# Performance work log

Hardware: AMD Instinct MI355X
Metric: run time of the kernel (lower is better)

## Reference

```python
import jax, jax.numpy as jnp
import numpy as np

N = 21  # nodes per graph (20 laser sectors + 1 robot node)
MAX_RANGE = 10.0
_bound = np.linspace(-np.pi / 2 - 0.03, np.pi / 2, 21, dtype=np.float32)[:-1]
_angles = _bound + np.float32(np.pi / 20)
ANGLE_FEAT = jnp.asarray(np.stack([np.sin(_angles), np.cos(_angles)], 1), dtype=jnp.float32)  # [20,2]


def _build_nodes(state24):
    # state24: [B,24] -> node features [B,21,7]
    B = state24.shape[0]
    laser = state24[:, :20, None] / MAX_RANGE                       # [B,20,1]
    angle = jnp.broadcast_to(ANGLE_FEAT[None], (B, 20, 2))          # [B,20,2]
    sector = jnp.concatenate([laser, angle, jnp.zeros((B, 20, 4), state24.dtype)], -1)  # [B,20,7]
    robot = jnp.concatenate([jnp.zeros((B, 1, 3), state24.dtype), state24[:, None, 20:]], -1)  # [B,1,7]
    return jnp.concatenate([sector, robot], axis=1)                 # [B,21,7]


def _gatv2(x, Wl, Wr, att, bias, heads, dim):
    # GATv2 over a fully-connected graph with self-loops (dense all-pairs).
    # e_ij = att . leaky_relu(Wl x_j + Wr x_i); alpha = softmax_j; out_i = sum_j alpha_ij (Wl x_j)
    B = x.shape[0]
    gl = (x @ Wl).reshape(B, N, heads, dim)  # source transform [B,j,H,D]
    gr = (x @ Wr).reshape(B, N, heads, dim)  # target transform [B,i,H,D]
    s = jax.nn.leaky_relu(gl[:, None] + gr[:, :, None], negative_slope=0.2)  # [B,i,j,H,D]
    e = jnp.einsum('bijhd,hd->bijh', s, att)                                  # [B,i,j,H]
    alpha = jax.nn.softmax(e, axis=2)                                          # softmax over sources j
    out = jnp.einsum('bijh,bjhd->bihd', alpha, gl).reshape(B, N, heads * dim)
    return out + bias


def setup_inputs() -> dict:
    key = jax.random.key(0)
    ks = jax.random.split(key, 16)
    r = lambda k, shape, s: (jax.random.normal(k, shape, dtype=jnp.float32) * s)
    B = 1024
    return {
        'state24': jax.random.normal(ks[0], (B, 24), dtype=jnp.float32),
        'Wl1': r(ks[1], (7, 256), 0.3), 'Wr1': r(ks[2], (7, 256), 0.3),
        'att1': r(ks[3], (4, 64), 0.1), 'b1': r(ks[4], (256,), 0.02),
        'Wl2': r(ks[5], (256, 64), 0.06), 'Wr2': r(ks[6], (256, 64), 0.06),
        'att2': r(ks[7], (1, 64), 0.1), 'b2': r(ks[8], (64,), 0.02),
        'fc1_w': r(ks[9], (64, 256), 0.12), 'fc1_b': r(ks[10], (256,), 0.02),
        'fc2_w': r(ks[11], (256, 256), 0.06), 'fc2_b': r(ks[12], (256,), 0.02),
        'fc3_w': r(ks[13], (256, 2), 0.06), 'fc3_b': r(ks[14], (2,), 0.02),
    }


def reference(state24, Wl1, Wr1, att1, b1, Wl2, Wr2, att2, b2,
              fc1_w, fc1_b, fc2_w, fc2_b, fc3_w, fc3_b):
    x = _build_nodes(state24)                               # [B,21,7]
    h = jax.nn.elu(_gatv2(x, Wl1, Wr1, att1, b1, 4, 64))    # [B,21,256]
    h = _gatv2(h, Wl2, Wr2, att2, b2, 1, 64)                # [B,21,64]
    nfv = jnp.mean(h, axis=1)                               # global_mean_pool -> [B,64]
    h = jax.nn.relu(nfv @ fc1_w + fc1_b)
    h = jax.nn.relu(h @ fc2_w + fc2_b)
    return jnp.tanh(h @ fc3_w + fc3_b)                      # [B,2]
```

## Files before the change

kernel.cpp:

```cpp
#include <hip/hip_runtime.h>
#include <hip/hip_fp16.h>
#include <math.h>

#define PI_D 3.141592653589793

typedef _Float16 h2 __attribute__((ext_vector_type(2)));
typedef _Float16 h4 __attribute__((ext_vector_type(4)));
typedef _Float16 h8 __attribute__((ext_vector_type(8)));
typedef unsigned short us8 __attribute__((ext_vector_type(8)));
typedef __fp16 f16v2 __attribute__((ext_vector_type(2)));
typedef __fp16 f16v8 __attribute__((ext_vector_type(8)));
typedef float f32x4 __attribute__((ext_vector_type(4)));

#define STR1 264
#define STR2H 72

static __device__ __forceinline__ h2 pack_h2(float a, float b) {
    return __builtin_bit_cast(h2, __builtin_amdgcn_cvt_pkrtz(a, b));
}

static __device__ __forceinline__ float fdot2(h2 a, h2 b, float c) {
    return __builtin_amdgcn_fdot2(__builtin_bit_cast(f16v2, a),
                                  __builtin_bit_cast(f16v2, b), c, false);
}

static __device__ __forceinline__ h8 habs8(h8 x) {
    us8 u = __builtin_bit_cast(us8, x);
    us8 m = {0x7fff, 0x7fff, 0x7fff, 0x7fff, 0x7fff, 0x7fff, 0x7fff, 0x7fff};
    return __builtin_bit_cast(h8, (us8)(u & m));
}

static __device__ __forceinline__ f32x4 mfma16(h8 a, h8 b, f32x4 c) {
    return __builtin_amdgcn_mfma_f32_16x16x32_f16(
        __builtin_bit_cast(f16v8, a), __builtin_bit_cast(f16v8, b), c, 0, 0, 0);
}

__global__ __launch_bounds__(256) void pack_weights_kernel(
    const float* __restrict__ Wl2, const float* __restrict__ Wr2,
    const float* __restrict__ fc1_w, const float* __restrict__ fc2_w,
    h8* __restrict__ ws)
{
    int idx = blockIdx.x * 256 + threadIdx.x;
    if (idx < 4096) {
        const float* W = idx < 2048 ? Wl2 : Wr2;
        int t = idx & 2047;
        int ntile = t >> 9, rem = t & 511;
        int kchunk = rem >> 6, lane = rem & 63;
        int n = ntile * 16 + (lane & 15);
        int k0 = kchunk * 32 + (lane >> 4) * 8;
        h8 o;
        #pragma unroll
        for (int j = 0; j < 8; ++j) o[j] = (_Float16)W[(k0 + j) * 64 + n];
        ws[idx] = o;
    } else if (idx < 6144) {
        int t = idx - 4096;
        int k2 = t >> 6, c = t & 63;
        h8 o;
        #pragma unroll
        for (int q = 0; q < 4; ++q) {
            o[2 * q]     = (_Float16)fc1_w[(2 * k2) * 256 + 4 * c + q];
            o[2 * q + 1] = (_Float16)fc1_w[(2 * k2 + 1) * 256 + 4 * c + q];
        }
        ws[idx] = o;
    } else {
        int t = idx - 6144;
        int k2 = t >> 6, c = t & 63;
        h8 o;
        #pragma unroll
        for (int q = 0; q < 4; ++q) {
            o[2 * q]     = (_Float16)fc2_w[(2 * k2) * 256 + 4 * c + q];
            o[2 * q + 1] = (_Float16)fc2_w[(2 * k2 + 1) * 256 + 4 * c + q];
        }
        ws[idx] = o;
    }
}

__global__ __launch_bounds__(256, 4) void actor_fused_kernel(
    const float* __restrict__ state24,
    const float* __restrict__ Wl1, const float* __restrict__ Wr1,
    const float* __restrict__ att1, const float* __restrict__ b1,
    const float* __restrict__ att2, const float* __restrict__ b2,
    const float* __restrict__ fc1_b, const float* __restrict__ fc2_b,
    const float* __restrict__ fc3_w, const float* __restrict__ fc3_b,
    const h8* __restrict__ wsL, const h8* __restrict__ wsR,
    const h8* __restrict__ wsF1, const h8* __restrict__ wsF2,
    float* __restrict__ out, int B)
{
    const int bix = blockIdx.x;
    if (bix >= B) return;
    const int tid = threadIdx.x;

    __shared__ float sinL[20], cosL[20], laserL[20], robotL[4];
    __shared__ __align__(16) h2 attLh[128];
    __shared__ __align__(16) h2 att2Lh[32];
    __shared__ __align__(16) _Float16 gr1h[22 * STR1];
    __shared__ __align__(16) union {
        struct { _Float16 gl1h[22 * STR1];
                 float ePf[128 * 24];
                 float uv[168]; } p1;
        struct { _Float16 gl2h[21 * STR2H];
                 _Float16 gr2h[21 * STR2H];
                 _Float16 gl2hT[64 * 32];
                 float e2[32 * 24];
                 float u2v2[42];
                 float red[4][256];
                 _Float16 nfvh[64]; _Float16 hah[256]; _Float16 hbh[256]; } p2;
    } U;

    if (tid < 20) {
        double step = (PI_D + 0.03) / 20.0;
        float bound = (float)(-PI_D / 2.0 - 0.03 + (double)tid * step);
        float ang = bound + (float)(PI_D / 20.0);
        sinL[tid] = sinf(ang);
        cosL[tid] = cosf(ang);
        laserL[tid] = state24[bix * 24 + tid] * 0.1f;
    }
    if (tid >= 32 && tid < 36) robotL[tid - 32] = state24[bix * 24 + 20 + (tid - 32)];
    if (tid < 128) {
        float2 ap = ((const float2*)att1)[tid];
        attLh[tid] = pack_h2(0.4f * ap.x, 0.4f * ap.y);
    }
    if (tid >= 128 && tid < 160) {
        float2 ap = ((const float2*)att2)[tid - 128];
        att2Lh[tid - 128] = pack_h2(0.4f * ap.x, 0.4f * ap.y);
    }
    __syncthreads();

    {
        h8 zz = {};
        if (tid < 33) ((h8*)U.p1.gl1h)[21 * 33 + tid] = zz;

        const int d2 = tid & 127;
        const int half = tid >> 7;
        float2 wl[7], wr[7];
        #pragma unroll
        for (int k = 0; k < 7; k++) {
            wl[k] = ((const float2*)Wl1)[k * 128 + d2];
            wr[k] = ((const float2*)Wr1)[k * 128 + d2];
        }
        const int base = half * 11;
        #pragma unroll
        for (int nn = 0; nn < 11; ++nn) {
            int node = base + nn;
            if (node < 21) {
                float a0, a1, b0, b1v;
                if (node < 20) {
                    float l = laserL[node], s = sinL[node], c = cosL[node];
                    a0 = l * wl[0].x + s * wl[1].x + c * wl[2].x;
                    a1 = l * wl[0].y + s * wl[1].y + c * wl[2].y;
                    b0 = l * wr[0].x + s * wr[1].x + c * wr[2].x;
                    b1v = l * wr[0].y + s * wr[1].y + c * wr[2].y;
                } else {
                    float r0 = robotL[0], r1 = robotL[1], r2 = robotL[2], r3 = robotL[3];
                    a0 = r0 * wl[3].x + r1 * wl[4].x + r2 * wl[5].x + r3 * wl[6].x;
                    a1 = r0 * wl[3].y + r1 * wl[4].y + r2 * wl[5].y + r3 * wl[6].y;
                    b0 = r0 * wr[3].x + r1 * wr[4].x + r2 * wr[5].x + r3 * wr[6].x;
                    b1v = r0 * wr[3].y + r1 * wr[4].y + r2 * wr[5].y + r3 * wr[6].y;
                }
                ((h2*)(U.p1.gl1h + node * STR1))[d2] = pack_h2(a0, a1);
                ((h2*)(gr1h + node * STR1))[d2] = pack_h2(b0, b1v);
            }
        }
    }
    __syncthreads();

    if (tid < 168) {
        int r = tid < 84 ? tid : tid - 84;
        int h = r / 21, idx = r - h * 21;
        const _Float16* rowp = (tid < 84 ? U.p1.gl1h : gr1h) + idx * STR1 + h * 64;
        const h8* row8 = (const h8*)rowp;
        const h2* ar = attLh + h * 32;
        float l0 = 0.f, l1 = 0.f;
        #pragma unroll
        for (int ch = 0; ch < 8; ++ch) {
            h8 g = row8[ch];
            l0 = fdot2(__builtin_shufflevector(g, g, 0, 1), ar[ch * 4 + 0], l0);
            l1 = fdot2(__builtin_shufflevector(g, g, 2, 3), ar[ch * 4 + 1], l1);
            l0 = fdot2(__builtin_shufflevector(g, g, 4, 5), ar[ch * 4 + 2], l0);
            l1 = fdot2(__builtin_shufflevector(g, g, 6, 7), ar[ch * 4 + 3], l1);
        }
        U.p1.uv[tid] = l0 + l1;
    }
    __syncthreads();

    {
        const int h = tid >> 6;
        const int lane = tid & 63;
        h2 ar[32];
        #pragma unroll
        for (int q = 0; q < 32; ++q) ar[q] = attLh[h * 32 + q];

        for (int it = 0; it < 7; ++it) {
            int q = it * 64 + lane;
            if (q < 441) {
                int i = q / 21;
                int j = q - i * 21;
                const h8* gA8 = (const h8*)(U.p1.gl1h + j * STR1 + h * 64);
                const h8* gB8 = (const h8*)(gr1h + i * STR1 + h * 64);
                float m0 = 0.f, m1 = 0.f;
                #pragma unroll
                for (int ch = 0; ch < 8; ++ch) {
                    h8 x = gA8[ch] + gB8[ch];
                    h8 ax = habs8(x);
                    m0 = fdot2(__builtin_shufflevector(ax, ax, 0, 1), ar[ch * 4 + 0], m0);
                    m1 = fdot2(__builtin_shufflevector(ax, ax, 2, 3), ar[ch * 4 + 1], m1);
                    m0 = fdot2(__builtin_shufflevector(ax, ax, 4, 5), ar[ch * 4 + 2], m0);
                    m1 = fdot2(__builtin_shufflevector(ax, ax, 6, 7), ar[ch * 4 + 3], m1);
                }
                U.p1.ePf[(h * 32 + i) * 24 + j] = m0 + m1;
            }
        }
    }
    __syncthreads();

    if (tid < 84) {
        int h = tid / 21, i = tid - h * 21;
        int r = h * 32 + i;
        float* row = U.p1.ePf + r * 24;
        const float* uu = U.p1.uv + h * 21;
        float vi = 1.5f * U.p1.uv[84 + h * 21 + i];
        float ebuf[21];
        float m = -1e30f;
        #pragma unroll
        for (int j = 0; j < 21; j++) {
            float e = row[j] + 1.5f * uu[j] + vi;
            ebuf[j] = e;
            m = fmaxf(m, e);
        }
        float s = 0.f;
        #pragma unroll
        for (int j = 0; j < 21; j++) { float v = __expf(ebuf[j] - m); ebuf[j] = v; s += v; }
        float rinv = 1.f / s;
        h8* hp8 = (h8*)(U.p1.ePf) + r * 6;
        h8 o0, o1, o2;
        #pragma unroll
        for (int q = 0; q < 8; ++q) o0[q] = (_Float16)(ebuf[q] * rinv);
        #pragma unroll
        for (int q = 0; q < 8; ++q) o1[q] = (_Float16)(ebuf[8 + q] * rinv);
        #pragma unroll
        for (int q = 0; q < 5; ++q) o2[q] = (_Float16)(ebuf[16 + q] * rinv);
        o2[5] = (_Float16)0.f; o2[6] = (_Float16)0.f; o2[7] = (_Float16)0.f;
        h8 zz = {};
        hp8[0] = o0; hp8[1] = o1; hp8[2] = o2;
        hp8[3] = zz; hp8[4] = zz; hp8[5] = zz;
    } else {
        h8 zz = {};
        for (int z = tid - 84; z < 264; z += 172) {
            int rr = z / 6, slot = z - rr * 6;
            int h = rr / 11, m = 21 + (rr - h * 11);
            ((h8*)U.p1.ePf)[(h * 32 + m) * 6 + slot] = zz;
        }
    }
    __syncthreads();

    {
        h8 zz = {};
        if (tid < 33) ((h8*)gr1h)[21 * 33 + tid] = zz;

        const int lane = tid & 63;
        const int h = tid >> 6;
        const int mcol = lane & 15;
        const int quad = lane >> 4;
        const h8* Af = (const h8*)U.p1.ePf;
        h8 A0 = Af[(h * 32 + mcol) * 6 + quad];
        h8 A1 = Af[(h * 32 + 16 + mcol) * 6 + quad];
        int rowoff[8];
        #pragma unroll
        for (int jj = 0; jj < 8; ++jj) {
            int rr = quad * 8 + jj;
            rowoff[jj] = (rr > 21 ? 21 : rr) * STR1;
        }
        const int colbase = h * 64 + mcol;
        f32x4 z4 = {0.f, 0.f, 0.f, 0.f};
        #pragma unroll
        for (int t = 0; t < 4; ++t) {
            int col = colbase + t * 16;
            h8 bv;
            #pragma unroll
            for (int jj = 0; jj < 8; ++jj) bv[jj] = U.p1.gl1h[rowoff[jj] + col];
            f32x4 d0 = mfma16(A0, bv, z4);
            f32x4 d1 = mfma16(A1, bv, z4);
            float bb = b1[col];
            #pragma unroll
            for (int r = 0; r < 4; ++r) {
                int n0 = quad * 4 + r;
                float v = d0[r] + bb;
                v = v > 0.f ? v : __expf(v) - 1.f;
                gr1h[n0 * STR1 + col] = (_Float16)v;
                int n1 = 16 + quad * 4 + r;
                if (n1 < 21) {
                    float w2 = d1[r] + bb;
                    w2 = w2 > 0.f ? w2 : __expf(w2) - 1.f;
                    gr1h[n1 * STR1 + col] = (_Float16)w2;
                }
            }
        }
    }
    __syncthreads();

    {
        const int lane = tid & 63;
        const int w = tid >> 6;
        const int mrow = lane & 15;
        const int quad = lane >> 4;
        int rowA1 = 16 + mrow; if (rowA1 > 21) rowA1 = 21;
        const h8* hA0 = (const h8*)(gr1h + mrow * STR1 + quad * 8);
        const h8* hA1 = (const h8*)(gr1h + rowA1 * STR1 + quad * 8);
        const h8* bL = wsL + w * 512 + lane;
        const h8* bR = wsR + w * 512 + lane;
        f32x4 aL0 = {0.f, 0.f, 0.f, 0.f}, aL1 = {0.f, 0.f, 0.f, 0.f};
        f32x4 aR0 = {0.f, 0.f, 0.f, 0.f}, aR1 = {0.f, 0.f, 0.f, 0.f};
        #pragma unroll
        for (int kc = 0; kc < 8; ++kc) {
            h8 A0 = hA0[kc * 4];
            h8 A1 = hA1[kc * 4];
            h8 BL = bL[kc * 64];
            h8 BR = bR[kc * 64];
            aL0 = mfma16(A0, BL, aL0);
            aL1 = mfma16(A1, BL, aL1);
            aR0 = mfma16(A0, BR, aR0);
            aR1 = mfma16(A1, BR, aR1);
        }
        const int col = w * 16 + mrow;
        #pragma unroll
        for (int r = 0; r < 4; ++r) {
            int row0 = quad * 4 + r;
            U.p2.gl2h[row0 * STR2H + col] = (_Float16)aL0[r];
            U.p2.gr2h[row0 * STR2H + col] = (_Float16)aR0[r];
            int row1 = 16 + row0;
            if (row1 < 21) {
                U.p2.gl2h[row1 * STR2H + col] = (_Float16)aL1[r];
                U.p2.gr2h[row1 * STR2H + col] = (_Float16)aR1[r];
            }
        }
        {
            h2 lo0 = pack_h2(aL0[0], aL0[1]);
            h2 hi0 = pack_h2(aL0[2], aL0[3]);
            h4 p0 = __builtin_shufflevector(lo0, hi0, 0, 1, 2, 3);
            *(h4*)(U.p2.gl2hT + col * 32 + quad * 4) = p0;
            float m0v = (16 + quad * 4 + 0 < 21) ? aL1[0] : 0.f;
            float m1v = (16 + quad * 4 + 1 < 21) ? aL1[1] : 0.f;
            float m2v = (16 + quad * 4 + 2 < 21) ? aL1[2] : 0.f;
            float m3v = (16 + quad * 4 + 3 < 21) ? aL1[3] : 0.f;
            h2 lo1 = pack_h2(m0v, m1v);
            h2 hi1 = pack_h2(m2v, m3v);
            h4 p1 = __builtin_shufflevector(lo1, hi1, 0, 1, 2, 3);
            *(h4*)(U.p2.gl2hT + col * 32 + 16 + quad * 4) = p1;
        }
    }
    __syncthreads();

    {
        h2 ar2[32];
        #pragma unroll
        for (int q = 0; q < 32; ++q) ar2[q] = att2Lh[q];

        #pragma unroll
        for (int it = 0; it < 2; ++it) {
            int t = it * 256 + tid;
            if (t < 441) {
                int i = t / 21;
                int j = t - i * 21;
                const h8* gA8 = (const h8*)(U.p2.gl2h + j * STR2H);
                const h8* gB8 = (const h8*)(U.p2.gr2h + i * STR2H);
                float m0 = 0.f, m1 = 0.f;
                #pragma unroll
                for (int ch = 0; ch < 8; ++ch) {
                    h8 x = gA8[ch] + gB8[ch];
                    h8 ax = habs8(x);
                    m0 = fdot2(__builtin_shufflevector(ax, ax, 0, 1), ar2[ch * 4 + 0], m0);
                    m1 = fdot2(__builtin_shufflevector(ax, ax, 2, 3), ar2[ch * 4 + 1], m1);
                    m0 = fdot2(__builtin_shufflevector(ax, ax, 4, 5), ar2[ch * 4 + 2], m0);
                    m1 = fdot2(__builtin_shufflevector(ax, ax, 6, 7), ar2[ch * 4 + 3], m1);
                }
                U.p2.e2[i * 24 + j] = m0 + m1;
            } else if (t < 483) {
                int u = t - 441;
                int r = u < 21 ? u : u - 21;
                const _Float16* rowp = (u < 21 ? U.p2.gl2h : U.p2.gr2h) + r * STR2H;
                const h8* row8 = (const h8*)rowp;
                float l0 = 0.f, l1 = 0.f;
                #pragma unroll
                for (int ch = 0; ch < 8; ++ch) {
                    h8 g = row8[ch];
                    l0 = fdot2(__builtin_shufflevector(g, g, 0, 1), ar2[ch * 4 + 0], l0);
                    l1 = fdot2(__builtin_shufflevector(g, g, 2, 3), ar2[ch * 4 + 1], l1);
                    l0 = fdot2(__builtin_shufflevector(g, g, 4, 5), ar2[ch * 4 + 2], l0);
                    l1 = fdot2(__builtin_shufflevector(g, g, 6, 7), ar2[ch * 4 + 3], l1);
                }
                U.p2.u2v2[u] = l0 + l1;
            }
        }
    }
    __syncthreads();

    if (tid < 21) {
        float* row = U.p2.e2 + tid * 24;
        const float* uu = U.p2.u2v2;
        float vi = 1.5f * U.p2.u2v2[21 + tid];
        float ebuf[21];
        float m = -1e30f;
        #pragma unroll
        for (int j = 0; j < 21; j++) {
            float e = row[j] + 1.5f * uu[j] + vi;
            ebuf[j] = e;
            m = fmaxf(m, e);
        }
        float s = 0.f;
        #pragma unroll
        for (int j = 0; j < 21; j++) { float v = __expf(ebuf[j] - m); ebuf[j] = v; s += v; }
        float rinv = 1.f / s;
        h8* hp8 = (h8*)(U.p2.e2) + tid * 6;
        h8 o0, o1, o2;
        #pragma unroll
        for (int q = 0; q < 8; ++q) o0[q] = (_Float16)(ebuf[q] * rinv);
        #pragma unroll
        for (int q = 0; q < 8; ++q) o1[q] = (_Float16)(ebuf[8 + q] * rinv);
        #pragma unroll
        for (int q = 0; q < 5; ++q) o2[q] = (_Float16)(ebuf[16 + q] * rinv);
        o2[5] = (_Float16)0.f; o2[6] = (_Float16)0.f; o2[7] = (_Float16)0.f;
        h8 zz = {};
        hp8[0] = o0; hp8[1] = o1; hp8[2] = o2;
        hp8[3] = zz; hp8[4] = zz; hp8[5] = zz;
    } else if (tid < 87) {
        int z = tid - 21;
        int rr = z / 6, slot = z - rr * 6;
        h8 zz = {};
        ((h8*)U.p2.e2)[(21 + rr) * 6 + slot] = zz;
    }
    __syncthreads();

    {
        const int lane = tid & 63;
        const int w = tid >> 6;
        const int mcol = lane & 15;
        const int quad = lane >> 4;
        const h8* Af2 = (const h8*)U.p2.e2;
        h8 A0 = Af2[mcol * 6 + quad];
        h8 A1 = Af2[(16 + mcol) * 6 + quad];
        h8 bv = *(const h8*)(U.p2.gl2hT + (w * 16 + mcol) * 32 + quad * 8);
        f32x4 z4 = {0.f, 0.f, 0.f, 0.f};
        f32x4 d0 = mfma16(A0, bv, z4);
        f32x4 d1 = mfma16(A1, bv, z4);
        float s = (d0[0] + d0[1]) + (d0[2] + d0[3])
                + (d1[0] + d1[1]) + (d1[2] + d1[3]);
        s += __shfl_xor(s, 16, 64);
        s += __shfl_xor(s, 32, 64);
        if (quad == 0) {
            int col = w * 16 + mcol;
            U.p2.nfvh[col] = (_Float16)(s * (1.f / 21.f) + b2[col]);
        }
    }
    __syncthreads();

    {
        int c = tid & 63, g = tid >> 6;
        const h2* x2p = (const h2*)U.p2.nfvh;
        float4 acc = {0.f, 0.f, 0.f, 0.f};
        #pragma unroll
        for (int kk = 0; kk < 8; ++kk) {
            int k2 = g * 8 + kk;
            h8 w = wsF1[k2 * 64 + c];
            h2 x2 = x2p[k2];
            acc.x = fdot2(__builtin_shufflevector(w, w, 0, 1), x2, acc.x);
            acc.y = fdot2(__builtin_shufflevector(w, w, 2, 3), x2, acc.y);
            acc.z = fdot2(__builtin_shufflevector(w, w, 4, 5), x2, acc.z);
            acc.w = fdot2(__builtin_shufflevector(w, w, 6, 7), x2, acc.w);
        }
        ((float4*)U.p2.red[g])[c] = acc;
    }
    __syncthreads();
    {
        float v = U.p2.red[0][tid] + U.p2.red[1][tid] + U.p2.red[2][tid] + U.p2.red[3][tid]
                  + fc1_b[tid];
        U.p2.hah[tid] = (_Float16)fmaxf(v, 0.f);
    }
    __syncthreads();

    {
        int c = tid & 63, g = tid >> 6;
        const h8* haH = (const h8*)U.p2.hah;
        float4 acc = {0.f, 0.f, 0.f, 0.f};
#define FC2_STEP(q, p)                                                          \
        {                                                                       \
            int k2 = g * 32 + (q) * 4 + (p);                                    \
            h8 w = wsF2[k2 * 64 + c];                                           \
            h2 x2 = __builtin_shufflevector(xa, xa, 2 * (p), 2 * (p) + 1);      \
            acc.x = fdot2(__builtin_shufflevector(w, w, 0, 1), x2, acc.x);      \
            acc.y = fdot2(__builtin_shufflevector(w, w, 2, 3), x2, acc.y);      \
            acc.z = fdot2(__builtin_shufflevector(w, w, 4, 5), x2, acc.z);      \
            acc.w = fdot2(__builtin_shufflevector(w, w, 6, 7), x2, acc.w);      \
        }
        #pragma unroll
        for (int q = 0; q < 8; ++q) {
            h8 xa = haH[g * 8 + q];
            FC2_STEP(q, 0)
            FC2_STEP(q, 1)
            FC2_STEP(q, 2)
            FC2_STEP(q, 3)
        }
#undef FC2_STEP
        ((float4*)U.p2.red[g])[c] = acc;
    }
    __syncthreads();
    {
        float v = U.p2.red[0][tid] + U.p2.red[1][tid] + U.p2.red[2][tid] + U.p2.red[3][tid]
                  + fc2_b[tid];
        U.p2.hbh[tid] = (_Float16)fmaxf(v, 0.f);
    }
    __syncthreads();

    if (tid < 128) {
        int o = tid >> 6, l = tid & 63;
        float s = 0.f;
        #pragma unroll
        for (int m = 0; m < 4; m++) {
            int k = l + 64 * m;
            s = fmaf((float)U.p2.hbh[k], fc3_w[k * 2 + o], s);
        }
        #pragma unroll
        for (int off = 32; off >= 1; off >>= 1) s += __shfl_down(s, off, 64);
        if (l == 0) out[bix * 2 + o] = tanhf(s + fc3_b[o]);
    }
}

extern "C" void kernel_launch(void* const* d_in, const int* in_sizes, int n_in,
                              void* d_out, int out_size, void* d_ws, size_t ws_size,
                              hipStream_t stream) {
    const float* state24 = (const float*)d_in[0];
    const float* Wl1 = (const float*)d_in[1];
    const float* Wr1 = (const float*)d_in[2];
    const float* att1 = (const float*)d_in[3];
    const float* b1 = (const float*)d_in[4];
    const float* Wl2 = (const float*)d_in[5];
    const float* Wr2 = (const float*)d_in[6];
    const float* att2 = (const float*)d_in[7];
    const float* b2 = (const float*)d_in[8];
    const float* fc1_w = (const float*)d_in[9];
    const float* fc1_b = (const float*)d_in[10];
    const float* fc2_w = (const float*)d_in[11];
    const float* fc2_b = (const float*)d_in[12];
    const float* fc3_w = (const float*)d_in[13];
    const float* fc3_b = (const float*)d_in[14];
    float* out = (float*)d_out;

    h8* ws = (h8*)d_ws;
    const h8* wsL = ws;
    const h8* wsR = ws + 2048;
    const h8* wsF1 = ws + 4096;
    const h8* wsF2 = ws + 6144;

    pack_weights_kernel<<<56, 256, 0, stream>>>(Wl2, Wr2, fc1_w, fc2_w, ws);

    int B = in_sizes[0] / 24;
    actor_fused_kernel<<<B, 256, 0, stream>>>(
        state24, Wl1, Wr1, att1, b1, att2, b2,
        fc1_b, fc2_b, fc3_w, fc3_b,
        wsL, wsR, wsF1, wsF2, out, B);
}
```

Before: 115.8 us.

## Restructure GAT layer-1 scoring, prefetch layer-2 weights, and make FC layers per-thread

Layer-1 pairwise attention scores are now computed by giving each lane one target node and seven source nodes, holding the target row in registers. The separate u/v projection pass is merged into the same barrier phase, which removes one __syncthreads. Padding rows are dropped (22→21 rows, 128→84 score rows), so several zero-fill passes go away, and the layer-2 weight fragments are loaded into registers before the MFMA stage. FC1 and FC2 weights are re-laid out so each thread computes one output column over the full K dimension. This removes the cross-group reduction buffer and two barriers, at the cost of more registers and longer per-thread dependency chains.

```diff
diff --git a/kernel.cpp b/kernel.cpp
--- a/kernel.cpp
+++ b/kernel.cpp
@@ -14,6 +14,8 @@
 
 #define STR1 264
 #define STR2H 72
+
+#define SV(v, a, b) __builtin_shufflevector(v, v, a, b)
 
 static __device__ __forceinline__ h2 pack_h2(float a, float b) {
     return __builtin_bit_cast(h2, __builtin_amdgcn_cvt_pkrtz(a, b));
@@ -54,23 +56,17 @@
         ws[idx] = o;
     } else if (idx < 6144) {
         int t = idx - 4096;
-        int k2 = t >> 6, c = t & 63;
+        int col = t >> 3, kk = t & 7;
         h8 o;
         #pragma unroll
-        for (int q = 0; q < 4; ++q) {
-            o[2 * q]     = (_Float16)fc1_w[(2 * k2) * 256 + 4 * c + q];
-            o[2 * q + 1] = (_Float16)fc1_w[(2 * k2 + 1) * 256 + 4 * c + q];
-        }
+        for (int j = 0; j < 8; ++j) o[j] = (_Float16)fc1_w[(kk * 8 + j) * 256 + col];
         ws[idx] = o;
     } else {
         int t = idx - 6144;
-        int k2 = t >> 6, c = t & 63;
+        int col = t >> 5, kk = t & 31;
         h8 o;
         #pragma unroll
-        for (int q = 0; q < 4; ++q) {
-            o[2 * q]     = (_Float16)fc2_w[(2 * k2) * 256 + 4 * c + q];
-            o[2 * q + 1] = (_Float16)fc2_w[(2 * k2 + 1) * 256 + 4 * c + q];
-        }
+        for (int j = 0; j < 8; ++j) o[j] = (_Float16)fc2_w[(kk * 8 + j) * 256 + col];
         ws[idx] = o;
     }
 }
@@ -93,17 +89,16 @@
     __shared__ float sinL[20], cosL[20], laserL[20], robotL[4];
     __shared__ __align__(16) h2 attLh[128];
     __shared__ __align__(16) h2 att2Lh[32];
-    __shared__ __align__(16) _Float16 gr1h[22 * STR1];
+    __shared__ __align__(16) _Float16 gr1h[21 * STR1];
     __shared__ __align__(16) union {
-        struct { _Float16 gl1h[22 * STR1];
-                 float ePf[128 * 24];
+        struct { _Float16 gl1h[21 * STR1];
+                 float ePf[84 * 24];
                  float uv[168]; } p1;
         struct { _Float16 gl2h[21 * STR2H];
                  _Float16 gr2h[21 * STR2H];
                  _Float16 gl2hT[64 * 32];
                  float e2[32 * 24];
                  float u2v2[42];
-                 float red[4][256];
                  _Float16 nfvh[64]; _Float16 hah[256]; _Float16 hbh[256]; } p2;
     } U;
 
@@ -127,9 +122,6 @@
     __syncthreads();
 
     {
-        h8 zz = {};
-        if (tid < 33) ((h8*)U.p1.gl1h)[21 * 33 + tid] = zz;
-
         const int d2 = tid & 127;
         const int half = tid >> 7;
         float2 wl[7], wr[7];
@@ -164,25 +156,6 @@
     }
     __syncthreads();
 
-    if (tid < 168) {
-        int r = tid < 84 ? tid : tid - 84;
-        int h = r / 21, idx = r - h * 21;
-        const _Float16* rowp = (tid < 84 ? U.p1.gl1h : gr1h) + idx * STR1 + h * 64;
-        const h8* row8 = (const h8*)rowp;
-        const h2* ar = attLh + h * 32;
-        float l0 = 0.f, l1 = 0.f;
-        #pragma unroll
-        for (int ch = 0; ch < 8; ++ch) {
-            h8 g = row8[ch];
-            l0 = fdot2(__builtin_shufflevector(g, g, 0, 1), ar[ch * 4 + 0], l0);
-            l1 = fdot2(__builtin_shufflevector(g, g, 2, 3), ar[ch * 4 + 1], l1);
-            l0 = fdot2(__builtin_shufflevector(g, g, 4, 5), ar[ch * 4 + 2], l0);
-            l1 = fdot2(__builtin_shufflevector(g, g, 6, 7), ar[ch * 4 + 3], l1);
-        }
-        U.p1.uv[tid] = l0 + l1;
-    }
-    __syncthreads();
-
     {
         const int h = tid >> 6;
         const int lane = tid & 63;
@@ -190,33 +163,54 @@
         #pragma unroll
         for (int q = 0; q < 32; ++q) ar[q] = attLh[h * 32 + q];
 
-        for (int it = 0; it < 7; ++it) {
-            int q = it * 64 + lane;
-            if (q < 441) {
-                int i = q / 21;
-                int j = q - i * 21;
-                const h8* gA8 = (const h8*)(U.p1.gl1h + j * STR1 + h * 64);
-                const h8* gB8 = (const h8*)(gr1h + i * STR1 + h * 64);
+        if (lane < 63) {
+            const int i = lane / 3;
+            const int jg = lane - i * 3;
+            const h8* gB8 = (const h8*)(gr1h + i * STR1 + h * 64);
+            h8 br[8];
+            #pragma unroll
+            for (int ch = 0; ch < 8; ++ch) br[ch] = gB8[ch];
+            const h8* gA8 = (const h8*)(U.p1.gl1h + (jg * 7) * STR1 + h * 64);
+            float* eo = U.p1.ePf + (h * 21 + i) * 24 + jg * 7;
+            #pragma unroll
+            for (int s = 0; s < 7; ++s) {
                 float m0 = 0.f, m1 = 0.f;
                 #pragma unroll
                 for (int ch = 0; ch < 8; ++ch) {
-                    h8 x = gA8[ch] + gB8[ch];
+                    h8 x = gA8[ch] + br[ch];
                     h8 ax = habs8(x);
-                    m0 = fdot2(__builtin_shufflevector(ax, ax, 0, 1), ar[ch * 4 + 0], m0);
-                    m1 = fdot2(__builtin_shufflevector(ax, ax, 2, 3), ar[ch * 4 + 1], m1);
-                    m0 = fdot2(__builtin_shufflevector(ax, ax, 4, 5), ar[ch * 4 + 2], m0);
-                    m1 = fdot2(__builtin_shufflevector(ax, ax, 6, 7), ar[ch * 4 + 3], m1);
+                    m0 = fdot2(SV(ax, 0, 1), ar[ch * 4 + 0], m0);
+                    m1 = fdot2(SV(ax, 2, 3), ar[ch * 4 + 1], m1);
+                    m0 = fdot2(SV(ax, 4, 5), ar[ch * 4 + 2], m0);
+                    m1 = fdot2(SV(ax, 6, 7), ar[ch * 4 + 3], m1);
                 }
-                U.p1.ePf[(h * 32 + i) * 24 + j] = m0 + m1;
+                eo[s] = m0 + m1;
+                gA8 += 33;
             }
+        }
+        if (tid < 168) {
+            int r = tid < 84 ? tid : tid - 84;
+            int hu = r / 21, idx = r - hu * 21;
+            const _Float16* rowp = (tid < 84 ? U.p1.gl1h : gr1h) + idx * STR1 + hu * 64;
+            const h8* row8 = (const h8*)rowp;
+            const h2* aru = attLh + hu * 32;
+            float l0 = 0.f, l1 = 0.f;
+            #pragma unroll
+            for (int ch = 0; ch < 8; ++ch) {
+                h8 g = row8[ch];
+                l0 = fdot2(SV(g, 0, 1), aru[ch * 4 + 0], l0);
+                l1 = fdot2(SV(g, 2, 3), aru[ch * 4 + 1], l1);
+                l0 = fdot2(SV(g, 4, 5), aru[ch * 4 + 2], l0);
+                l1 = fdot2(SV(g, 6, 7), aru[ch * 4 + 3], l1);
+            }
+            U.p1.uv[tid] = l0 + l1;
         }
     }
     __syncthreads();
 
     if (tid < 84) {
         int h = tid / 21, i = tid - h * 21;
-        int r = h * 32 + i;
-        float* row = U.p1.ePf + r * 24;
+        float* row = U.p1.ePf + tid * 24;
         const float* uu = U.p1.uv + h * 21;
         float vi = 1.5f * U.p1.uv[84 + h * 21 + i];
         float ebuf[21];
@@ -231,7 +225,7 @@
         #pragma unroll
         for (int j = 0; j < 21; j++) { float v = __expf(ebuf[j] - m); ebuf[j] = v; s += v; }
         float rinv = 1.f / s;
-        h8* hp8 = (h8*)(U.p1.ePf) + r * 6;
+        h8* hp8 = (h8*)(U.p1.ePf) + tid * 6;
         h8 o0, o1, o2;
         #pragma unroll
         for (int q = 0; q < 8; ++q) o0[q] = (_Float16)(ebuf[q] * rinv);
@@ -243,32 +237,30 @@
         h8 zz = {};
         hp8[0] = o0; hp8[1] = o1; hp8[2] = o2;
         hp8[3] = zz; hp8[4] = zz; hp8[5] = zz;
-    } else {
-        h8 zz = {};
-        for (int z = tid - 84; z < 264; z += 172) {
-            int rr = z / 6, slot = z - rr * 6;
-            int h = rr / 11, m = 21 + (rr - h * 11);
-            ((h8*)U.p1.ePf)[(h * 32 + m) * 6 + slot] = zz;
-        }
-    }
-    __syncthreads();
-
-    {
-        h8 zz = {};
-        if (tid < 33) ((h8*)gr1h)[21 * 33 + tid] = zz;
-
+    }
+    __syncthreads();
+
+    h8 pbL[8], pbR[8];
+    {
         const int lane = tid & 63;
-        const int h = tid >> 6;
+        const int w = tid >> 6;
+        const h8* bLp = wsL + w * 512 + lane;
+        const h8* bRp = wsR + w * 512 + lane;
+        #pragma unroll
+        for (int kc = 0; kc < 8; ++kc) { pbL[kc] = bLp[kc * 64]; pbR[kc] = bRp[kc * 64]; }
+
+        const int h = w;
         const int mcol = lane & 15;
         const int quad = lane >> 4;
         const h8* Af = (const h8*)U.p1.ePf;
-        h8 A0 = Af[(h * 32 + mcol) * 6 + quad];
-        h8 A1 = Af[(h * 32 + 16 + mcol) * 6 + quad];
+        h8 A0 = Af[(h * 21 + mcol) * 6 + quad];
+        int m1r = 16 + mcol; if (m1r > 20) m1r = 20;
+        h8 A1 = Af[(h * 21 + m1r) * 6 + quad];
         int rowoff[8];
         #pragma unroll
         for (int jj = 0; jj < 8; ++jj) {
             int rr = quad * 8 + jj;
-            rowoff[jj] = (rr > 21 ? 21 : rr) * STR1;
+            rowoff[jj] = (rr > 20 ? 20 : rr) * STR1;
         }
         const int colbase = h * 64 + mcol;
         f32x4 z4 = {0.f, 0.f, 0.f, 0.f};
@@ -303,23 +295,19 @@
         const int w = tid >> 6;
         const int mrow = lane & 15;
         const int quad = lane >> 4;
-        int rowA1 = 16 + mrow; if (rowA1 > 21) rowA1 = 21;
+        int rowA1 = 16 + mrow; if (rowA1 > 20) rowA1 = 20;
         const h8* hA0 = (const h8*)(gr1h + mrow * STR1 + quad * 8);
         const h8* hA1 = (const h8*)(gr1h + rowA1 * STR1 + quad * 8);
-        const h8* bL = wsL + w * 512 + lane;
-        const h8* bR = wsR + w * 512 + lane;
         f32x4 aL0 = {0.f, 0.f, 0.f, 0.f}, aL1 = {0.f, 0.f, 0.f, 0.f};
         f32x4 aR0 = {0.f, 0.f, 0.f, 0.f}, aR1 = {0.f, 0.f, 0.f, 0.f};
         #pragma unroll
         for (int kc = 0; kc < 8; ++kc) {
             h8 A0 = hA0[kc * 4];
             h8 A1 = hA1[kc * 4];
-            h8 BL = bL[kc * 64];
-            h8 BR = bR[kc * 64];
-            aL0 = mfma16(A0, BL, aL0);
-            aL1 = mfma16(A1, BL, aL1);
-            aR0 = mfma16(A0, BR, aR0);
-            aR1 = mfma16(A1, BR, aR1);
+            aL0 = mfma16(A0, pbL[kc], aL0);
+            aL1 = mfma16(A1, pbL[kc], aL1);
+            aR0 = mfma16(A0, pbR[kc], aR0);
+            aR1 = mfma16(A1, pbR[kc], aR1);
         }
         const int col = w * 16 + mrow;
         #pragma unroll
@@ -338,12 +326,8 @@
             h2 hi0 = pack_h2(aL0[2], aL0[3]);
             h4 p0 = __builtin_shufflevector(lo0, hi0, 0, 1, 2, 3);
             *(h4*)(U.p2.gl2hT + col * 32 + quad * 4) = p0;
-            float m0v = (16 + quad * 4 + 0 < 21) ? aL1[0] : 0.f;
-            float m1v = (16 + quad * 4 + 1 < 21) ? aL1[1] : 0.f;
-            float m2v = (16 + quad * 4 + 2 < 21) ? aL1[2] : 0.f;
-            float m3v = (16 + quad * 4 + 3 < 21) ? aL1[3] : 0.f;
-            h2 lo1 = pack_h2(m0v, m1v);
-            h2 hi1 = pack_h2(m2v, m3v);
+            h2 lo1 = pack_h2(aL1[0], aL1[1]);
+            h2 hi1 = pack_h2(aL1[2], aL1[3]);
             h4 p1 = __builtin_shufflevector(lo1, hi1, 0, 1, 2, 3);
             *(h4*)(U.p2.gl2hT + col * 32 + 16 + quad * 4) = p1;
         }
@@ -368,10 +352,10 @@
                 for (int ch = 0; ch < 8; ++ch) {
                     h8 x = gA8[ch] + gB8[ch];
                     h8 ax = habs8(x);
-                    m0 = fdot2(__builtin_shufflevector(ax, ax, 0, 1), ar2[ch * 4 + 0], m0);
-                    m1 = fdot2(__builtin_shufflevector(ax, ax, 2, 3), ar2[ch * 4 + 1], m1);
-                    m0 = fdot2(__builtin_shufflevector(ax, ax, 4, 5), ar2[ch * 4 + 2], m0);
-                    m1 = fdot2(__builtin_shufflevector(ax, ax, 6, 7), ar2[ch * 4 + 3], m1);
+                    m0 = fdot2(SV(ax, 0, 1), ar2[ch * 4 + 0], m0);
+                    m1 = fdot2(SV(ax, 2, 3), ar2[ch * 4 + 1], m1);
+                    m0 = fdot2(SV(ax, 4, 5), ar2[ch * 4 + 2], m0);
+                    m1 = fdot2(SV(ax, 6, 7), ar2[ch * 4 + 3], m1);
                 }
                 U.p2.e2[i * 24 + j] = m0 + m1;
             } else if (t < 483) {
@@ -383,10 +367,10 @@
                 #pragma unroll
                 for (int ch = 0; ch < 8; ++ch) {
                     h8 g = row8[ch];
-                    l0 = fdot2(__builtin_shufflevector(g, g, 0, 1), ar2[ch * 4 + 0], l0);
-                    l1 = fdot2(__builtin_shufflevector(g, g, 2, 3), ar2[ch * 4 + 1], l1);
-                    l0 = fdot2(__builtin_shufflevector(g, g, 4, 5), ar2[ch * 4 + 2], l0);
-                    l1 = fdot2(__builtin_shufflevector(g, g, 6, 7), ar2[ch * 4 + 3], l1);
+                    l0 = fdot2(SV(g, 0, 1), ar2[ch * 4 + 0], l0);
+                    l1 = fdot2(SV(g, 2, 3), ar2[ch * 4 + 1], l1);
+                    l0 = fdot2(SV(g, 4, 5), ar2[ch * 4 + 2], l0);
+                    l1 = fdot2(SV(g, 6, 7), ar2[ch * 4 + 3], l1);
                 }
                 U.p2.u2v2[u] = l0 + l1;
             }
@@ -454,58 +438,40 @@
     __syncthreads();
 
     {
-        int c = tid & 63, g = tid >> 6;
-        const h2* x2p = (const h2*)U.p2.nfvh;
-        float4 acc = {0.f, 0.f, 0.f, 0.f};
+        const h8* nf8 = (const h8*)U.p2.nfvh;
+        h8 xv[8];
+        #pragma unroll
+        for (int q = 0; q < 8; ++q) xv[q] = nf8[q];
+        const h8* wp = wsF1 + tid * 8;
+        float a0 = 0.f, a1 = 0.f, a2 = 0.f, a3 = 0.f;
         #pragma unroll
         for (int kk = 0; kk < 8; ++kk) {
-            int k2 = g * 8 + kk;
-            h8 w = wsF1[k2 * 64 + c];
-            h2 x2 = x2p[k2];
-            acc.x = fdot2(__builtin_shufflevector(w, w, 0, 1), x2, acc.x);
-            acc.y = fdot2(__builtin_shufflevector(w, w, 2, 3), x2, acc.y);
-            acc.z = fdot2(__builtin_shufflevector(w, w, 4, 5), x2, acc.z);
-            acc.w = fdot2(__builtin_shufflevector(w, w, 6, 7), x2, acc.w);
-        }
-        ((float4*)U.p2.red[g])[c] = acc;
-    }
-    __syncthreads();
-    {
-        float v = U.p2.red[0][tid] + U.p2.red[1][tid] + U.p2.red[2][tid] + U.p2.red[3][tid]
-                  + fc1_b[tid];
+            h8 w = wp[kk];
+            h8 xa = xv[kk];
+            a0 = fdot2(SV(w, 0, 1), SV(xa, 0, 1), a0);
+            a1 = fdot2(SV(w, 2, 3), SV(xa, 2, 3), a1);
+            a2 = fdot2(SV(w, 4, 5), SV(xa, 4, 5), a2);
+            a3 = fdot2(SV(w, 6, 7), SV(xa, 6, 7), a3);
+        }
+        float v = (a0 + a1) + (a2 + a3) + fc1_b[tid];
         U.p2.hah[tid] = (_Float16)fmaxf(v, 0.f);
     }
     __syncthreads();
 
     {
-        int c = tid & 63, g = tid >> 6;
-        const h8* haH = (const h8*)U.p2.hah;
-        float4 acc = {0.f, 0.f, 0.f, 0.f};
-#define FC2_STEP(q, p)                                                          \
-        {                                                                       \
-            int k2 = g * 32 + (q) * 4 + (p);                                    \
-            h8 w = wsF2[k2 * 64 + c];                                           \
-            h2 x2 = __builtin_shufflevector(xa, xa, 2 * (p), 2 * (p) + 1);      \
-            acc.x = fdot2(__builtin_shufflevector(w, w, 0, 1), x2, acc.x);      \
-            acc.y = fdot2(__builtin_shufflevector(w, w, 2, 3), x2, acc.y);      \
-            acc.z = fdot2(__builtin_shufflevector(w, w, 4, 5), x2, acc.z);      \
-            acc.w = fdot2(__builtin_shufflevector(w, w, 6, 7), x2, acc.w);      \
-        }
-        #pragma unroll
-        for (int q = 0; q < 8; ++q) {
-            h8 xa = haH[g * 8 + q];
-            FC2_STEP(q, 0)
-            FC2_STEP(q, 1)
-            FC2_STEP(q, 2)
-            FC2_STEP(q, 3)
-        }
-#undef FC2_STEP
-        ((float4*)U.p2.red[g])[c] = acc;
-    }
-    __syncthreads();
-    {
-        float v = U.p2.red[0][tid] + U.p2.red[1][tid] + U.p2.red[2][tid] + U.p2.red[3][tid]
-                  + fc2_b[tid];
+        const h8* ha8 = (const h8*)U.p2.hah;
+        const h8* wp = wsF2 + tid * 32;
+        float a0 = 0.f, a1 = 0.f, a2 = 0.f, a3 = 0.f;
+        #pragma unroll
+        for (int q8 = 0; q8 < 32; ++q8) {
+            h8 xa = ha8[q8];
+            h8 w = wp[q8];
+            a0 = fdot2(SV(w, 0, 1), SV(xa, 0, 1), a0);
+            a1 = fdot2(SV(w, 2, 3), SV(xa, 2, 3), a1);
+            a2 = fdot2(SV(w, 4, 5), SV(xa, 4, 5), a2);
+            a3 = fdot2(SV(w, 6, 7), SV(xa, 6, 7), a3);
+        }
+        float v = (a0 + a1) + (a2 + a3) + fc2_b[tid];
         U.p2.hbh[tid] = (_Float16)fmaxf(v, 0.f);
     }
     __syncthreads();
```

New measurement: 127.1 us. 1.1x slower.

## Make layer-1 GATv2 head-local per wave and replace block barriers with wave fences

Applied to the files above, without the earlier changes.

Reassigns the layer-1 work so each wave handles one attention head end to end: the input projection for that head's columns, the pairwise scores, the per-node attention terms, the softmax and the MFMA aggregation. Because the data a wave produces is then read only by that same wave, four block-wide __syncthreads are replaced with wave-level fences, aiming to cut barrier stalls and idle threads between phases. The padding zeroing is redistributed per head, and the masking of padded rows in the layer-2 transpose is dropped, which relies on those rows being zero. The correctness of the fences depends on LDS ordering within a wave, and the padded-row assumption is a risk.

```diff
diff --git a/kernel.cpp b/kernel.cpp
--- a/kernel.cpp
+++ b/kernel.cpp
@@ -15,6 +15,8 @@
 #define STR1 264
 #define STR2H 72
 
+#define SV(v, a, b) __builtin_shufflevector(v, v, a, b)
+
 static __device__ __forceinline__ h2 pack_h2(float a, float b) {
     return __builtin_bit_cast(h2, __builtin_amdgcn_cvt_pkrtz(a, b));
 }
@@ -33,6 +35,14 @@
 static __device__ __forceinline__ f32x4 mfma16(h8 a, h8 b, f32x4 c) {
     return __builtin_amdgcn_mfma_f32_16x16x32_f16(
         __builtin_bit_cast(f16v8, a), __builtin_bit_cast(f16v8, b), c, 0, 0, 0);
+}
+
+static __device__ __forceinline__ void wave_fence() {
+    asm volatile("" ::: "memory");
+#if __has_builtin(__builtin_amdgcn_wave_barrier)
+    __builtin_amdgcn_wave_barrier();
+#endif
+    asm volatile("" ::: "memory");
 }
 
 __global__ __launch_bounds__(256) void pack_weights_kernel(
@@ -127,171 +137,169 @@
     __syncthreads();
 
     {
-        h8 zz = {};
-        if (tid < 33) ((h8*)U.p1.gl1h)[21 * 33 + tid] = zz;
-
-        const int d2 = tid & 127;
-        const int half = tid >> 7;
-        float2 wl[7], wr[7];
-        #pragma unroll
-        for (int k = 0; k < 7; k++) {
-            wl[k] = ((const float2*)Wl1)[k * 128 + d2];
-            wr[k] = ((const float2*)Wr1)[k * 128 + d2];
-        }
-        const int base = half * 11;
-        #pragma unroll
-        for (int nn = 0; nn < 11; ++nn) {
-            int node = base + nn;
-            if (node < 21) {
-                float a0, a1, b0, b1v;
-                if (node < 20) {
-                    float l = laserL[node], s = sinL[node], c = cosL[node];
-                    a0 = l * wl[0].x + s * wl[1].x + c * wl[2].x;
-                    a1 = l * wl[0].y + s * wl[1].y + c * wl[2].y;
-                    b0 = l * wr[0].x + s * wr[1].x + c * wr[2].x;
-                    b1v = l * wr[0].y + s * wr[1].y + c * wr[2].y;
-                } else {
-                    float r0 = robotL[0], r1 = robotL[1], r2 = robotL[2], r3 = robotL[3];
-                    a0 = r0 * wl[3].x + r1 * wl[4].x + r2 * wl[5].x + r3 * wl[6].x;
-                    a1 = r0 * wl[3].y + r1 * wl[4].y + r2 * wl[5].y + r3 * wl[6].y;
-                    b0 = r0 * wr[3].x + r1 * wr[4].x + r2 * wr[5].x + r3 * wr[6].x;
-                    b1v = r0 * wr[3].y + r1 * wr[4].y + r2 * wr[5].y + r3 * wr[6].y;
-                }
-                ((h2*)(U.p1.gl1h + node * STR1))[d2] = pack_h2(a0, a1);
-                ((h2*)(gr1h + node * STR1))[d2] = pack_h2(b0, b1v);
-            }
-        }
-    }
-    __syncthreads();
-
-    if (tid < 168) {
-        int r = tid < 84 ? tid : tid - 84;
-        int h = r / 21, idx = r - h * 21;
-        const _Float16* rowp = (tid < 84 ? U.p1.gl1h : gr1h) + idx * STR1 + h * 64;
-        const h8* row8 = (const h8*)rowp;
-        const h2* ar = attLh + h * 32;
-        float l0 = 0.f, l1 = 0.f;
-        #pragma unroll
-        for (int ch = 0; ch < 8; ++ch) {
-            h8 g = row8[ch];
-            l0 = fdot2(__builtin_shufflevector(g, g, 0, 1), ar[ch * 4 + 0], l0);
-            l1 = fdot2(__builtin_shufflevector(g, g, 2, 3), ar[ch * 4 + 1], l1);
-            l0 = fdot2(__builtin_shufflevector(g, g, 4, 5), ar[ch * 4 + 2], l0);
-            l1 = fdot2(__builtin_shufflevector(g, g, 6, 7), ar[ch * 4 + 3], l1);
-        }
-        U.p1.uv[tid] = l0 + l1;
-    }
-    __syncthreads();
-
-    {
         const int h = tid >> 6;
         const int lane = tid & 63;
-        h2 ar[32];
-        #pragma unroll
-        for (int q = 0; q < 32; ++q) ar[q] = attLh[h * 32 + q];
-
-        for (int it = 0; it < 7; ++it) {
-            int q = it * 64 + lane;
-            if (q < 441) {
-                int i = q / 21;
-                int j = q - i * 21;
-                const h8* gA8 = (const h8*)(U.p1.gl1h + j * STR1 + h * 64);
-                const h8* gB8 = (const h8*)(gr1h + i * STR1 + h * 64);
-                float m0 = 0.f, m1 = 0.f;
+
+        {
+            const int cp = lane & 31;
+            const int half = lane >> 5;
+            const int d2 = h * 32 + cp;
+            float2 wl[7], wr[7];
+            #pragma unroll
+            for (int k = 0; k < 7; k++) {
+                wl[k] = ((const float2*)Wl1)[k * 128 + d2];
+                wr[k] = ((const float2*)Wr1)[k * 128 + d2];
+            }
+            if (half == 0) {
+                h2 zz2 = {};
+                ((h2*)(U.p1.gl1h + 21 * STR1))[d2] = zz2;
+                ((h2*)(gr1h + 21 * STR1))[d2] = zz2;
+            }
+            const int base = half * 11;
+            #pragma unroll
+            for (int nn = 0; nn < 11; ++nn) {
+                int node = base + nn;
+                if (node < 21) {
+                    float a0, a1, b0, b1v;
+                    if (node < 20) {
+                        float l = laserL[node], s = sinL[node], c = cosL[node];
+                        a0 = l * wl[0].x + s * wl[1].x + c * wl[2].x;
+                        a1 = l * wl[0].y + s * wl[1].y + c * wl[2].y;
+                        b0 = l * wr[0].x + s * wr[1].x + c * wr[2].x;
+                        b1v = l * wr[0].y + s * wr[1].y + c * wr[2].y;
+                    } else {
+                        float r0 = robotL[0], r1 = robotL[1], r2 = robotL[2], r3 = robotL[3];
+                        a0 = r0 * wl[3].x + r1 * wl[4].x + r2 * wl[5].x + r3 * wl[6].x;
+                        a1 = r0 * wl[3].y + r1 * wl[4].y + r2 * wl[5].y + r3 * wl[6].y;
+                        b0 = r0 * wr[3].x + r1 * wr[4].x + r2 * wr[5].x + r3 * wr[6].x;
+                        b1v = r0 * wr[3].y + r1 * wr[4].y + r2 * wr[5].y + r3 * wr[6].y;
+                    }
+                    ((h2*)(U.p1.gl1h + node * STR1))[d2] = pack_h2(a0, a1);
+                    ((h2*)(gr1h + node * STR1))[d2] = pack_h2(b0, b1v);
+                }
+            }
+        }
+        wave_fence();
+
+        {
+            h2 ar[32];
+            #pragma unroll
+            for (int q = 0; q < 32; ++q) ar[q] = attLh[h * 32 + q];
+
+            for (int it = 0; it < 7; ++it) {
+                int q = it * 64 + lane;
+                if (q < 441) {
+                    int i = q / 21;
+                    int j = q - i * 21;
+                    const h8* gA8 = (const h8*)(U.p1.gl1h + j * STR1 + h * 64);
+                    const h8* gB8 = (const h8*)(gr1h + i * STR1 + h * 64);
+                    float m0 = 0.f, m1 = 0.f;
+                    #pragma unroll
+                    for (int ch = 0; ch < 8; ++ch) {
+                        h8 x = gA8[ch] + gB8[ch];
+                        h8 ax = habs8(x);
+                        m0 = fdot2(SV(ax, 0, 1), ar[ch * 4 + 0], m0);
+                        m1 = fdot2(SV(ax, 2, 3), ar[ch * 4 + 1], m1);
+                        m0 = fdot2(SV(ax, 4, 5), ar[ch * 4 + 2], m0);
+                        m1 = fdot2(SV(ax, 6, 7), ar[ch * 4 + 3], m1);
+                    }
+                    U.p1.ePf[(h * 32 + i) * 24 + j] = m0 + m1;
+                }
+            }
+            if (lane < 42) {
+                int isV = lane >= 21;
+                int idx = isV ? lane - 21 : lane;
+                const _Float16* rowp = (isV ? (const _Float16*)gr1h
+                                            : (const _Float16*)U.p1.gl1h) + idx * STR1 + h * 64;
+                const h8* row8 = (const h8*)rowp;
+                float l0 = 0.f, l1 = 0.f;
                 #pragma unroll
                 for (int ch = 0; ch < 8; ++ch) {
-                    h8 x = gA8[ch] + gB8[ch];
-                    h8 ax = habs8(x);
-                    m0 = fdot2(__builtin_shufflevector(ax, ax, 0, 1), ar[ch * 4 + 0], m0);
-                    m1 = fdot2(__builtin_shufflevector(ax, ax, 2, 3), ar[ch * 4 + 1], m1);
-                    m0 = fdot2(__builtin_shufflevector(ax, ax, 4, 5), ar[ch * 4 + 2], m0);
-                    m1 = fdot2(__builtin_shufflevector(ax, ax, 6, 7), ar[ch * 4 + 3], m1);
+                    h8 g = row8[ch];
+                    l0 = fdot2(SV(g, 0, 1), ar[ch * 4 + 0], l0);
+                    l1 = fdot2(SV(g, 2, 3), ar[ch * 4 + 1], l1);
+                    l0 = fdot2(SV(g, 4, 5), ar[ch * 4 + 2], l0);
+                    l1 = fdot2(SV(g, 6, 7), ar[ch * 4 + 3], l1);
                 }
-                U.p1.ePf[(h * 32 + i) * 24 + j] = m0 + m1;
-            }
-        }
-    }
-    __syncthreads();
-
-    if (tid < 84) {
-        int h = tid / 21, i = tid - h * 21;
-        int r = h * 32 + i;
-        float* row = U.p1.ePf + r * 24;
-        const float* uu = U.p1.uv + h * 21;
-        float vi = 1.5f * U.p1.uv[84 + h * 21 + i];
-        float ebuf[21];
-        float m = -1e30f;
-        #pragma unroll
-        for (int j = 0; j < 21; j++) {
-            float e = row[j] + 1.5f * uu[j] + vi;
-            ebuf[j] = e;
-            m = fmaxf(m, e);
-        }
-        float s = 0.f;
-        #pragma unroll
-        for (int j = 0; j < 21; j++) { float v = __expf(ebuf[j] - m); ebuf[j] = v; s += v; }
-        float rinv = 1.f / s;
-        h8* hp8 = (h8*)(U.p1.ePf) + r * 6;
-        h8 o0, o1, o2;
-        #pragma unroll
-        for (int q = 0; q < 8; ++q) o0[q] = (_Float16)(ebuf[q] * rinv);
-        #pragma unroll
-        for (int q = 0; q < 8; ++q) o1[q] = (_Float16)(ebuf[8 + q] * rinv);
-        #pragma unroll
-        for (int q = 0; q < 5; ++q) o2[q] = (_Float16)(ebuf[16 + q] * rinv);
-        o2[5] = (_Float16)0.f; o2[6] = (_Float16)0.f; o2[7] = (_Float16)0.f;
-        h8 zz = {};
-        hp8[0] = o0; hp8[1] = o1; hp8[2] = o2;
-        hp8[3] = zz; hp8[4] = zz; hp8[5] = zz;
-    } else {
-        h8 zz = {};
-        for (int z = tid - 84; z < 264; z += 172) {
-            int rr = z / 6, slot = z - rr * 6;
-            int h = rr / 11, m = 21 + (rr - h * 11);
-            ((h8*)U.p1.ePf)[(h * 32 + m) * 6 + slot] = zz;
-        }
-    }
-    __syncthreads();
-
-    {
-        h8 zz = {};
-        if (tid < 33) ((h8*)gr1h)[21 * 33 + tid] = zz;
-
-        const int lane = tid & 63;
-        const int h = tid >> 6;
-        const int mcol = lane & 15;
-        const int quad = lane >> 4;
-        const h8* Af = (const h8*)U.p1.ePf;
-        h8 A0 = Af[(h * 32 + mcol) * 6 + quad];
-        h8 A1 = Af[(h * 32 + 16 + mcol) * 6 + quad];
-        int rowoff[8];
-        #pragma unroll
-        for (int jj = 0; jj < 8; ++jj) {
-            int rr = quad * 8 + jj;
-            rowoff[jj] = (rr > 21 ? 21 : rr) * STR1;
-        }
-        const int colbase = h * 64 + mcol;
-        f32x4 z4 = {0.f, 0.f, 0.f, 0.f};
-        #pragma unroll
-        for (int t = 0; t < 4; ++t) {
-            int col = colbase + t * 16;
-            h8 bv;
-            #pragma unroll
-            for (int jj = 0; jj < 8; ++jj) bv[jj] = U.p1.gl1h[rowoff[jj] + col];
-            f32x4 d0 = mfma16(A0, bv, z4);
-            f32x4 d1 = mfma16(A1, bv, z4);
-            float bb = b1[col];
-            #pragma unroll
-            for (int r = 0; r < 4; ++r) {
-                int n0 = quad * 4 + r;
-                float v = d0[r] + bb;
-                v = v > 0.f ? v : __expf(v) - 1.f;
-                gr1h[n0 * STR1 + col] = (_Float16)v;
-                int n1 = 16 + quad * 4 + r;
-                if (n1 < 21) {
-                    float w2 = d1[r] + bb;
-                    w2 = w2 > 0.f ? w2 : __expf(w2) - 1.f;
-                    gr1h[n1 * STR1 + col] = (_Float16)w2;
+                U.p1.uv[(isV ? 84 : 0) + h * 21 + idx] = l0 + l1;
+            }
+        }
+        wave_fence();
+
+        if (lane < 21) {
+            int r = h * 32 + lane;
+            float* row = U.p1.ePf + r * 24;
+            const float* uu = U.p1.uv + h * 21;
+            float vi = 1.5f * U.p1.uv[84 + h * 21 + lane];
+            float ebuf[21];
+            float m = -1e30f;
+            #pragma unroll
+            for (int j = 0; j < 21; j++) {
+                float e = row[j] + 1.5f * uu[j] + vi;
+                ebuf[j] = e;
+                m = fmaxf(m, e);
+            }
+            float s = 0.f;
+            #pragma unroll
+            for (int j = 0; j < 21; j++) { float v = __expf(ebuf[j] - m); ebuf[j] = v; s += v; }
+            float rinv = 1.f / s;
+            h8* hp8 = (h8*)(U.p1.ePf) + r * 6;
+            h8 o0, o1, o2;
+            #pragma unroll
+            for (int q = 0; q < 8; ++q) o0[q] = (_Float16)(ebuf[q] * rinv);
+            #pragma unroll
+            for (int q = 0; q < 8; ++q) o1[q] = (_Float16)(ebuf[8 + q] * rinv);
+            #pragma unroll
+            for (int q = 0; q < 5; ++q) o2[q] = (_Float16)(ebuf[16 + q] * rinv);
+            o2[5] = (_Float16)0.f; o2[6] = (_Float16)0.f; o2[7] = (_Float16)0.f;
+            h8 zz = {};
+            hp8[0] = o0; hp8[1] = o1; hp8[2] = o2;
+            hp8[3] = zz; hp8[4] = zz; hp8[5] = zz;
+        }
+        {
+            h8 zz = {};
+            for (int z = lane; z < 66; z += 64) {
+                int rr = z / 6, slot = z - rr * 6;
+                ((h8*)U.p1.ePf)[(h * 32 + 21 + rr) * 6 + slot] = zz;
+            }
+        }
+        wave_fence();
+
+        {
+            const int mcol = lane & 15;
+            const int quad = lane >> 4;
+            const h8* Af = (const h8*)U.p1.ePf;
+            h8 A0 = Af[(h * 32 + mcol) * 6 + quad];
+            h8 A1 = Af[(h * 32 + 16 + mcol) * 6 + quad];
+            int rowoff[8];
+            #pragma unroll
+            for (int jj = 0; jj < 8; ++jj) {
+                int rr = quad * 8 + jj;
+                rowoff[jj] = (rr > 21 ? 21 : rr) * STR1;
+            }
+            const int colbase = h * 64 + mcol;
+            f32x4 z4 = {0.f, 0.f, 0.f, 0.f};
+            #pragma unroll
+            for (int t = 0; t < 4; ++t) {
+                int col = colbase + t * 16;
+                h8 bv;
+                #pragma unroll
+                for (int jj = 0; jj < 8; ++jj) bv[jj] = U.p1.gl1h[rowoff[jj] + col];
+                f32x4 d0 = mfma16(A0, bv, z4);
+                f32x4 d1 = mfma16(A1, bv, z4);
+                float bb = b1[col];
+                #pragma unroll
+                for (int r = 0; r < 4; ++r) {
+                    int n0 = quad * 4 + r;
+                    float v = d0[r] + bb;
+                    v = v > 0.f ? v : __expf(v) - 1.f;
+                    gr1h[n0 * STR1 + col] = (_Float16)v;
+                    int n1 = 16 + quad * 4 + r;
+                    if (n1 < 21) {
+                        float w2 = d1[r] + bb;
+                        w2 = w2 > 0.f ? w2 : __expf(w2) - 1.f;
+                        gr1h[n1 * STR1 + col] = (_Float16)w2;
+                    }
                 }
             }
         }
@@ -338,12 +346,8 @@
             h2 hi0 = pack_h2(aL0[2], aL0[3]);
             h4 p0 = __builtin_shufflevector(lo0, hi0, 0, 1, 2, 3);
             *(h4*)(U.p2.gl2hT + col * 32 + quad * 4) = p0;
-            float m0v = (16 + quad * 4 + 0 < 21) ? aL1[0] : 0.f;
-            float m1v = (16 + quad * 4 + 1 < 21) ? aL1[1] : 0.f;
-            float m2v = (16 + quad * 4 + 2 < 21) ? aL1[2] : 0.f;
-            float m3v = (16 + quad * 4 + 3 < 21) ? aL1[3] : 0.f;
-            h2 lo1 = pack_h2(m0v, m1v);
-            h2 hi1 = pack_h2(m2v, m3v);
+            h2 lo1 = pack_h2(aL1[0], aL1[1]);
+            h2 hi1 = pack_h2(aL1[2], aL1[3]);
             h4 p1 = __builtin_shufflevector(lo1, hi1, 0, 1, 2, 3);
             *(h4*)(U.p2.gl2hT + col * 32 + 16 + quad * 4) = p1;
         }
@@ -368,10 +372,10 @@
                 for (int ch = 0; ch < 8; ++ch) {
                     h8 x = gA8[ch] + gB8[ch];
                     h8 ax = habs8(x);
-                    m0 = fdot2(__builtin_shufflevector(ax, ax, 0, 1), ar2[ch * 4 + 0], m0);
-                    m1 = fdot2(__builtin_shufflevector(ax, ax, 2, 3), ar2[ch * 4 + 1], m1);
-                    m0 = fdot2(__builtin_shufflevector(ax, ax, 4, 5), ar2[ch * 4 + 2], m0);
-                    m1 = fdot2(__builtin_shufflevector(ax, ax, 6, 7), ar2[ch * 4 + 3], m1);
+                    m0 = fdot2(SV(ax, 0, 1), ar2[ch * 4 + 0], m0);
+                    m1 = fdot2(SV(ax, 2, 3), ar2[ch * 4 + 1], m1);
+                    m0 = fdot2(SV(ax, 4, 5), ar2[ch * 4 + 2], m0);
+                    m1 = fdot2(SV(ax, 6, 7), ar2[ch * 4 + 3], m1);
                 }
                 U.p2.e2[i * 24 + j] = m0 + m1;
             } else if (t < 483) {
@@ -383,10 +387,10 @@
                 #pragma unroll
                 for (int ch = 0; ch < 8; ++ch) {
                     h8 g = row8[ch];
-                    l0 = fdot2(__builtin_shufflevector(g, g, 0, 1), ar2[ch * 4 + 0], l0);
-                    l1 = fdot2(__builtin_shufflevector(g, g, 2, 3), ar2[ch * 4 + 1], l1);
-                    l0 = fdot2(__builtin_shufflevector(g, g, 4, 5), ar2[ch * 4 + 2], l0);
-                    l1 = fdot2(__builtin_shufflevector(g, g, 6, 7), ar2[ch * 4 + 3], l1);
+                    l0 = fdot2(SV(g, 0, 1), ar2[ch * 4 + 0], l0);
+                    l1 = fdot2(SV(g, 2, 3), ar2[ch * 4 + 1], l1);
+                    l0 = fdot2(SV(g, 4, 5), ar2[ch * 4 + 2], l0);
+                    l1 = fdot2(SV(g, 6, 7), ar2[ch * 4 + 3], l1);
                 }
                 U.p2.u2v2[u] = l0 + l1;
             }
@@ -462,10 +466,10 @@
             int k2 = g * 8 + kk;
             h8 w = wsF1[k2 * 64 + c];
             h2 x2 = x2p[k2];
-            acc.x = fdot2(__builtin_shufflevector(w, w, 0, 1), x2, acc.x);
-            acc.y = fdot2(__builtin_shufflevector(w, w, 2, 3), x2, acc.y);
-            acc.z = fdot2(__builtin_shufflevector(w, w, 4, 5), x2, acc.z);
-            acc.w = fdot2(__builtin_shufflevector(w, w, 6, 7), x2, acc.w);
+            acc.x = fdot2(SV(w, 0, 1), x2, acc.x);
+            acc.y = fdot2(SV(w, 2, 3), x2, acc.y);
+            acc.z = fdot2(SV(w, 4, 5), x2, acc.z);
+            acc.w = fdot2(SV(w, 6, 7), x2, acc.w);
         }
         ((float4*)U.p2.red[g])[c] = acc;
     }
@@ -486,10 +490,10 @@
             int k2 = g * 32 + (q) * 4 + (p);                                    \
             h8 w = wsF2[k2 * 64 + c];                                           \
             h2 x2 = __builtin_shufflevector(xa, xa, 2 * (p), 2 * (p) + 1);      \
-            acc.x = fdot2(__builtin_shufflevector(w, w, 0, 1), x2, acc.x);      \
-            acc.y = fdot2(__builtin_shufflevector(w, w, 2, 3), x2, acc.y);      \
-            acc.z = fdot2(__builtin_shufflevector(w, w, 4, 5), x2, acc.z);      \
-            acc.w = fdot2(__builtin_shufflevector(w, w, 6, 7), x2, acc.w);      \
+            acc.x = fdot2(SV(w, 0, 1), x2, acc.x);                              \
+            acc.y = fdot2(SV(w, 2, 3), x2, acc.y);                              \
+            acc.z = fdot2(SV(w, 4, 5), x2, acc.z);                              \
+            acc.w = fdot2(SV(w, 6, 7), x2, acc.w);                              \
         }
         #pragma unroll
         for (int q = 0; q < 8; ++q) {
```

New measurement: 113.6 us. Within noise of the previous version (-1.9%).
